# Kernel optimization log

Hardware: AMD Instinct MI355X
Metric: run time of the kernel (lower is better)

Reference implementation:

```python
import jax, jax.numpy as jnp
import numpy as np

INF = jnp.float32(1e9)  # sentinel; true costs are O(10)


def _hungarian_cost(cost):
    """Exact min-cost perfect matching total cost (Jonker-Volgenant potentials
    algorithm, O(n^3)), matching scipy.optimize.linear_sum_assignment.
    cost: (n, n) float32 -> scalar sum of matched costs."""
    n = cost.shape[0]
    # pad with dummy row/col 0 (1-indexed algorithm)
    a = jnp.zeros((n + 1, n + 1), cost.dtype).at[1:, 1:].set(cost)

    def row_step(carry, i):
        u, v, p = carry  # u,v: dual potentials; p[j] = row matched to col j
        p = p.at[0].set(i)
        minv = jnp.full(n + 1, INF, cost.dtype)
        used = jnp.zeros(n + 1, bool)
        way = jnp.zeros(n + 1, jnp.int32)

        def cond(st):
            u, v, p, minv, used, way, j0, first = st
            return first | (p[j0] != 0)

        def body(st):
            u, v, p, minv, used, way, j0, _ = st
            used = used.at[j0].set(True)
            i0 = p[j0]
            cur = a[i0] - u[i0] - v                      # reduced costs of row i0
            upd = (~used) & (cur < minv)
            way = jnp.where(upd, j0, way)
            minv = jnp.where(upd, cur, minv)
            masked = jnp.where(used, INF, minv)
            j1 = jnp.argmin(masked).astype(jnp.int32)
            delta = masked[j1]
            # u[p[j]] += delta for used j (unused scatter adds 0, harmless)
            u = u.at[p].add(jnp.where(used, delta, 0.0))
            v = jnp.where(used, v - delta, v)
            minv = jnp.where(used, minv, minv - delta)
            return (u, v, p, minv, used, way, j1, False)

        u, v, p, minv, used, way, j0, _ = jax.lax.while_loop(
            cond, body, (u, v, p, minv, used, way, jnp.int32(0), True))

        # augment along alternating path
        def aug_body(st):
            p, j0 = st
            j1 = way[j0]
            return p.at[j0].set(p[j1]), j1

        p, _ = jax.lax.while_loop(lambda st: st[1] != 0, aug_body, (p, j0))
        return (u, v, p), None

    init = (jnp.zeros(n + 1, cost.dtype),
            jnp.zeros(n + 1, cost.dtype),
            jnp.zeros(n + 1, jnp.int32))
    (u, v, p), _ = jax.lax.scan(row_step, init,
                                jnp.arange(1, n + 1, dtype=jnp.int32))
    cols = jnp.arange(1, n + 1)
    return a[p[1:], cols].sum()


def setup_inputs() -> dict:
    key = jax.random.key(0)
    k1, k2 = jax.random.split(key)
    B, N = 8, 1024
    S1 = jax.random.normal(k1, (B, N, 3), dtype=jnp.float32)
    S2 = jax.random.normal(k2, (B, N, 3), dtype=jnp.float32)
    return {"S1": S1, "S2": S2}


def reference(S1, S2):
    B, N, _ = S1.shape
    # torch.cdist(p=2): per-sample pairwise Euclidean distances -> (B, N, N)
    diff = S1[:, :, None, :] - S2[:, None, :, :]
    cost = jnp.sqrt(jnp.sum(diff * diff, axis=-1))
    per_sample = jax.vmap(_hungarian_cost)(cost) / N  # optimal assignment cost / N
    return jnp.mean(per_sample)
```

## Files before the change

kernel.cpp:

```cpp
#include <hip/hip_runtime.h>
#include <hip/hip_fp16.h>
#include <math.h>


#define N     1024
#define BATCH 8
#define NSLOT 16
#define INFV  1e9f
#define AUC_ROUNDS 48

__global__ void emd_zero_kernel(float* out) { out[0] = 0.0f; }

__global__ __launch_bounds__(256)
void emd_dist_kernel(const float* __restrict__ S1, const float* __restrict__ S2,
                     __half* __restrict__ D) {
    int b = blockIdx.x >> 10;
    int r = blockIdx.x & (N - 1);
    const float* s1 = S1 + ((size_t)b * N + r) * 3;
    float x1 = s1[0], y1 = s1[1], z1 = s1[2];
    const float* s2 = S2 + (size_t)b * N * 3;
    __half* drow = D + ((size_t)b * N + r) * (size_t)N;
    for (int c = threadIdx.x; c < N; c += 256) {
        float dx = x1 - s2[3 * c], dy = y1 - s2[3 * c + 1], dz = z1 - s2[3 * c + 2];
        drow[c] = __float2half_rn(sqrtf(dx * dx + dy * dy + dz * dz));
    }
}

__global__ __launch_bounds__(256)
void emd_colmin_kernel(const __half* __restrict__ D, float* __restrict__ V,
                       int* __restrict__ I) {
    int b = blockIdx.x >> 2;
    int c = ((blockIdx.x & 3) << 8) + threadIdx.x;
    const __half* Db = D + ((size_t)b << 20);
    float best = INFV; int bi = 1;
    for (int r = 0; r < N; ++r) {
        float d = __half2float(Db[(size_t)r * N + c]);
        if (d < best) { best = d; bi = r + 1; }
    }
    V[b * N + c] = best;
    I[b * N + c] = bi;
}

template<int CTRL>
__device__ __forceinline__ float dppmin(float x) {
    int xi = __float_as_int(x);
    int yi = __builtin_amdgcn_update_dpp(xi, xi, CTRL, 0xF, 0xF, false);
    return fminf(x, __int_as_float(yi));
}

__device__ __forceinline__ float wave_min_f32(float x) {
    x = dppmin<0x111>(x);
    x = dppmin<0x112>(x);
    x = dppmin<0x114>(x);
    x = dppmin<0x118>(x);
    x = dppmin<0x142>(x);
    x = dppmin<0x143>(x);
    return __int_as_float(__builtin_amdgcn_readlane(__float_as_int(x), 63));
}

__global__ __launch_bounds__(1024, 1)
void emd_auction_kernel(const __half* __restrict__ Dc,
                        const float* __restrict__ Vin,
                        const int* __restrict__ Iin,
                        float* __restrict__ Vw, float* __restrict__ Uw,
                        int* __restrict__ Cw, int* __restrict__ Rw) {
    __shared__ float v0[N];
    __shared__ int   rowm[N + 1];
    __shared__ int   colm[N + 1];
    __shared__ unsigned long long bid[N + 1];
    __shared__ int   qbuf[N];
    __shared__ int   qn;

    const int tid  = threadIdx.x;
    const int lane = tid & 63;
    const int wv   = tid >> 6;
    const int b    = blockIdx.x;
    const __half* Db = Dc + ((size_t)b << 20);

    for (int t = tid; t <= N; t += 1024) { rowm[t] = 0; colm[t] = 0; bid[t] = 0ull; }
    for (int c = tid; c < N; c += 1024) v0[c] = Vin[b * N + c];
    __syncthreads();

    for (int c = tid; c < N; c += 1024) {
        int r = Iin[b * N + c];
        int old = atomicCAS(&rowm[r], 0, c + 1);
        if (old == 0) colm[c + 1] = r;
    }
    __syncthreads();

    auto rowRed16 = [&](int i, float (&red)[16]) {
        const uint4* dr = (const uint4*)(Db + (size_t)(i - 1) * N);
        uint4 w0 = dr[lane * 2 + 0];
        uint4 w1 = dr[lane * 2 + 1];
        unsigned wb[8] = { w0.x, w0.y, w0.z, w0.w, w1.x, w1.y, w1.z, w1.w };
        const float4* vp = (const float4*)(v0 + lane * 16);
        float4 vv0 = vp[0], vv1 = vp[1], vv2 = vp[2], vv3 = vp[3];
        float vv[16] = { vv0.x, vv0.y, vv0.z, vv0.w, vv1.x, vv1.y, vv1.z, vv1.w,
                         vv2.x, vv2.y, vv2.z, vv2.w, vv3.x, vv3.y, vv3.z, vv3.w };
#pragma unroll
        for (int t = 0; t < 8; ++t) {
            __half2 hh = *reinterpret_cast<const __half2*>(&wb[t]);
            float2 f2 = __half22float2(hh);
            red[2 * t]     = f2.x - vv[2 * t];
            red[2 * t + 1] = f2.y - vv[2 * t + 1];
        }
    };

    for (int round = 0; round < AUC_ROUNDS; ++round) {
        if (tid == 0) qn = 0;
        __syncthreads();
        for (int i = tid + 1; i <= N; i += 1024)
            if (rowm[i] == 0) { int p = atomicAdd(&qn, 1); qbuf[p] = i; }
        __syncthreads();
        int nq = qn;
        if (nq == 0) break;

        for (int q = wv; q < nq; q += 16) {
            int i = qbuf[q];
            float red[16];
            rowRed16(i, red);
            float a1 = INFV, a2 = INFV; int ac = 0;
            float e1 = INFV, e2 = INFV; int ec = 0;
            float f1 = INFV, f2 = INFV; int fc = 0;
            float g1 = INFV, g2 = INFV; int gc = 0;
#pragma unroll
            for (int k = 0; k < 4; ++k) {
                float u0 = red[k];
                bool t0 = u0 < a1;
                a2 = t0 ? a1 : (u0 < a2 ? u0 : a2);
                ac = t0 ? (lane * 16 + k) : ac;  a1 = t0 ? u0 : a1;
                float u1 = red[k + 4];
                bool t1 = u1 < e1;
                e2 = t1 ? e1 : (u1 < e2 ? u1 : e2);
                ec = t1 ? (lane * 16 + k + 4) : ec;  e1 = t1 ? u1 : e1;
                float u2 = red[k + 8];
                bool t2 = u2 < f1;
                f2 = t2 ? f1 : (u2 < f2 ? u2 : f2);
                fc = t2 ? (lane * 16 + k + 8) : fc;  f1 = t2 ? u2 : f1;
                float u3 = red[k + 12];
                bool t3 = u3 < g1;
                g2 = t3 ? g1 : (u3 < g2 ? u3 : g2);
                gc = t3 ? (lane * 16 + k + 12) : gc;  g1 = t3 ? u3 : g1;
            }
            bool sae = e1 < a1;
            float ae1 = sae ? e1 : a1; int aec = sae ? ec : ac;
            float ae2 = fminf(fminf(a2, e2), sae ? a1 : e1);
            bool sfg = g1 < f1;
            float fg1 = sfg ? g1 : f1; int fgc = sfg ? gc : fc;
            float fg2 = fminf(fminf(f2, g2), sfg ? f1 : g1);
            bool sall = fg1 < ae1;
            float m1 = sall ? fg1 : ae1;
            int   c1 = sall ? fgc : aec;
            float m2 = fminf(fminf(ae2, fg2), sall ? ae1 : fg1);

            float gm1 = wave_min_f32(m1);
            unsigned long long wbm = __ballot(m1 == gm1);
            int wl = __ffsll((long long)wbm) - 1;
            float cand2 = (lane == wl) ? m2 : m1;
            float gm2 = wave_min_f32(cand2);
            int gcol;
            if (gm1 < gm2) {
                gcol = __builtin_amdgcn_readlane(c1, wl);
            } else {
                unsigned tmask = 0u;
#pragma unroll
                for (int k = 0; k < 16; ++k)
                    tmask |= (red[k] == gm1) ? (1u << k) : 0u;
                unsigned fmask = 0u;
                unsigned tt = tmask;
                while (tt) {
                    int k = __ffs((int)tt) - 1;
                    tt &= tt - 1;
                    if (colm[lane * 16 + k + 1] == 0) fmask |= (1u << k);
                }
                unsigned long long bf = __ballot(fmask != 0u);
                if (bf != 0ull) {
                    int l = __ffsll((long long)bf) - 1;
                    unsigned mk = (unsigned)__builtin_amdgcn_readlane((int)fmask, l);
                    gcol = l * 16 + (__ffs((int)mk) - 1);
                } else {
                    gcol = __builtin_amdgcn_readlane(c1, wl);
                }
            }
            float inc = gm2 - gm1;

            if (lane == 0) {
                unsigned long long key =
                    ((unsigned long long)__float_as_uint(inc) << 32) |
                    (unsigned long long)(unsigned)i;
                atomicMax(&bid[gcol + 1], key);
            }
        }
        __syncthreads();

        for (int j = tid + 1; j <= N; j += 1024) {
            unsigned long long bb = bid[j];
            if (bb != 0ull) {
                bid[j] = 0ull;
                int i = (int)(unsigned)(bb & 0xFFFFFFFFull);
                float inc = __uint_as_float((unsigned)(bb >> 32));
                int old = colm[j];
                colm[j] = i;
                rowm[i] = j;
                if (old) rowm[old] = 0;
                v0[j - 1] -= inc;
            }
        }
        __syncthreads();
    }

    for (int q = wv; q < N; q += 16) {
        int i = q + 1;
        float red[16];
        rowRed16(i, red);
        int j = rowm[i];
        float rloc = red[0];
        int lo = 0, kk = 0;
        if (j) {
            lo = (j - 1) >> 4; kk = (j - 1) & 15;
#pragma unroll
            for (int k = 1; k < 16; ++k) if (k == kk) rloc = red[k];
        }
#pragma unroll
        for (int s = 1; s < 16; s <<= 1) {
#pragma unroll
            for (int k = 0; k < 16; k += 2 * s)
                red[k] = fminf(red[k], red[k + s]);
        }
        float m = wave_min_f32(red[0]);
        if (j) {
            float rm = __int_as_float(
                __builtin_amdgcn_readlane(__float_as_int(rloc), lo));
            if (lane == 0 && rm != m) { rowm[i] = 0; colm[j] = 0; }
        }
        if (lane == 0) Uw[b * N + q] = m;
    }
    __syncthreads();

    for (int c = tid; c < N; c += 1024) {
        Vw[b * N + c] = v0[c];
        Cw[b * N + c] = colm[c + 1];
    }
    for (int t = tid; t < N; t += 1024) Rw[b * N + t] = rowm[t + 1];
}

struct Frag { uint4 w0, w1; float ur; float4 q; };

template<bool CACHED, bool PRE>
__global__ __launch_bounds__(64, 1)
void emd_jv_kernel(const float* __restrict__ S1,
                   const float* __restrict__ S2,
                   const __half* __restrict__ Dc,
                   const float* __restrict__ Vin,
                   const int*   __restrict__ Iin,
                   const float* __restrict__ Uw,
                   const int*   __restrict__ Cw,
                   const int*   __restrict__ Rw,
                   float* __restrict__ out) {
    __shared__ float4 s1u[N + 1];
    __shared__ float  u_lds[N + 1];
    __shared__ float  dentry[N + 1];
    __shared__ int    rowm[N + 1];

    const int lane = threadIdx.x;
    const int b = blockIdx.x;
    const float* s1g = S1 + (size_t)b * N * 3;
    const float* s2g = S2 + (size_t)b * N * 3;
    const __half* Db = CACHED ? (Dc + ((size_t)b << 20)) : (const __half*)0;
    const float NANF = __int_as_float(0x7fc00000);

    for (int t = lane; t < N; t += 64) {
        s1u[t + 1] = make_float4(s1g[3 * t], s1g[3 * t + 1], s1g[3 * t + 2], 0.0f);
        u_lds[t + 1] = PRE ? Uw[b * N + t] : 0.0f;
        rowm[t + 1] = PRE ? Rw[b * N + t] : 0;
    }
    if (lane == 0) { u_lds[0] = 0.0f; rowm[0] = 0; }

    float v[NSLOT];
    int   pr[NSLOT];
    int   jpk[NSLOT];
    float x2[NSLOT], y2[NSLOT], z2[NSLOT];

#pragma unroll
    for (int k = 0; k < NSLOT; ++k) {
        int pt = lane * NSLOT + k;
        x2[k] = s2g[3 * pt + 0];
        y2[k] = s2g[3 * pt + 1];
        z2[k] = s2g[3 * pt + 2];
    }

    if constexpr (PRE) {
#pragma unroll
        for (int k = 0; k < NSLOT; ++k) {
            int c = lane * NSLOT + k;
            v[k] = Vin[b * N + c];
            pr[k] = Cw[b * N + c];
            jpk[k] = (pr[k] << 11) | (c + 1);
        }
        __syncthreads();
    } else {
        int imin[NSLOT];
        if constexpr (CACHED) {
#pragma unroll
            for (int k = 0; k < NSLOT; ++k) {
                int c = lane * NSLOT + k;
                v[k] = Vin[b * N + c];
                imin[k] = Iin[b * N + c];
            }
        } else {
#pragma unroll
            for (int k = 0; k < NSLOT; ++k) { v[k] = INFV; imin[k] = 1; }
        }
        __syncthreads();

        if constexpr (!CACHED) {
            for (int r = 1; r <= N; ++r) {
                float4 qq = s1u[r];
#pragma unroll
                for (int k = 0; k < NSLOT; ++k) {
                    float dx = qq.x - x2[k], dy = qq.y - y2[k], dz = qq.z - z2[k];
                    float d2 = dx * dx + dy * dy + dz * dz;
                    bool upd = d2 < v[k];
                    v[k] = upd ? d2 : v[k];
                    imin[k] = upd ? r : imin[k];
                }
            }
#pragma unroll
            for (int k = 0; k < NSLOT; ++k) v[k] = sqrtf(v[k]);
        }

#pragma unroll
        for (int k = 0; k < NSLOT; ++k) {
            int j = lane * NSLOT + k + 1;
            int r = imin[k];
            int old = atomicCAS(&rowm[r], 0, j);
            pr[k] = (old == 0) ? r : 0;
            jpk[k] = (pr[k] << 11) | j;
        }
        __syncthreads();
    }

    float minv[NSLOT];
    int   way[NSLOT];

    auto issueLoads = [&](int rr) -> Frag {
        Frag F;
        if (CACHED) {
            const uint4* dr = (const uint4*)(Db + (size_t)(rr - 1) * N);
            F.w0 = dr[lane * 2 + 0];
            F.w1 = dr[lane * 2 + 1];
        } else {
            F.q = s1u[rr];
        }
        F.ur = u_lds[rr];
        return F;
    };

    auto applyFrag = [&](const Frag& F, int jpred, float Dh) {
        float base = Dh - F.ur;
        if (CACHED) {
            float h[NSLOT];
            const unsigned* w = (const unsigned*)&F.w0;
#pragma unroll
            for (int t = 0; t < 8; ++t) {
                unsigned word = w[t];
                __half2 hh = *reinterpret_cast<const __half2*>(&word);
                float2 f2 = __half22float2(hh);
                h[2 * t] = f2.x; h[2 * t + 1] = f2.y;
            }
#pragma unroll
            for (int k = 0; k < NSLOT; ++k) {
                float cur = (h[k] - v[k]) + base;
                bool upd = cur < minv[k];
                minv[k] = upd ? cur : minv[k];
                way[k] = upd ? jpred : way[k];
            }
        } else {
#pragma unroll
            for (int k = 0; k < NSLOT; ++k) {
                float dx = F.q.x - x2[k], dy = F.q.y - y2[k], dz = F.q.z - z2[k];
                float d = sqrtf(dx * dx + dy * dy + dz * dz);
                float cur = (d - v[k]) + base;
                bool upd = cur < minv[k];
                minv[k] = upd ? cur : minv[k];
                way[k] = upd ? jpred : way[k];
            }
        }
    };

    for (int i = 1; i <= N; ++i) {
        if (rowm[i] != 0) continue;

        unsigned used = 0u;
        float DT = 0.0f;
        int freecol = 0;
        int pred = 0;
        Frag P;

        Frag F0 = issueLoads(i);
#pragma unroll
        for (int k = 0; k < NSLOT; ++k) { minv[k] = INFV; way[k] = 0; }
        applyFrag(F0, 0, 0.0f);

        int guard = 0;
        for (;;) {
            if (++guard > N + 4) break;
            float b0 = INFV, b1 = INFV, b2 = INFV, b3 = INFV;
            int   p0 = 0, p1 = 0, p2 = 0, p3 = 0;
#pragma unroll
            for (int k = 0; k < 4; ++k) {
                bool t0 = minv[k]      < b0;
                b0 = t0 ? minv[k]      : b0;  p0 = t0 ? jpk[k]      : p0;
                bool t1 = minv[k + 4]  < b1;
                b1 = t1 ? minv[k + 4]  : b1;  p1 = t1 ? jpk[k + 4]  : p1;
                bool t2 = minv[k + 8]  < b2;
                b2 = t2 ? minv[k + 8]  : b2;  p2 = t2 ? jpk[k + 8]  : p2;
                bool t3 = minv[k + 12] < b3;
                b3 = t3 ? minv[k + 12] : b3;  p3 = t3 ? jpk[k + 12] : p3;
            }
            bool m01 = b1 < b0;  float ba = m01 ? b1 : b0;  int pa = m01 ? p1 : p0;
            bool m23 = b3 < b2;  float bb = m23 ? b3 : b2;  int pb = m23 ? p3 : p2;
            bool mab = bb < ba;  float bestv = mab ? bb : ba;
            int bestjp = mab ? pb : pa;

            float gmin = wave_min_f32(bestv);
            if (!(gmin < INFV * 0.5f)) break;
            unsigned long long tm = __ballot(bestv == gmin);
            DT = gmin;
            freecol = 0;

            {
                unsigned long long tf = tm;
                while (tf) {
                    int l = __ffsll((long long)tf) - 1;
                    tf &= tf - 1;
                    int jp = __builtin_amdgcn_readlane(bestjp, l);
                    if ((jp >> 11) == 0) { freecol = jp & 0x7FF; break; }
                }
            }
            if (freecol) break;

            bool first = true;
            while (tm) {
                int l = __ffsll((long long)tm) - 1;
                tm &= tm - 1;
                int jp = __builtin_amdgcn_readlane(bestjp, l);
                int jj = jp & 0x7FF, rr = jp >> 11;
                Frag F;
                if (CACHED && first && pred != 0 && rr == pred) {
                    F = P;
                } else {
                    F = issueLoads(rr);
                }
                if (CACHED && first) {
                    float ru = (bestv == gmin) ? INFV : bestv;
                    float rmin = wave_min_f32(ru);
                    pred = 0;
                    if (rmin < INFV * 0.5f) {
                        unsigned long long rb = __ballot(ru == rmin);
                        int rl = __ffsll((long long)rb) - 1;
                        int rjp = __builtin_amdgcn_readlane(bestjp, rl);
                        int prr = rjp >> 11;
                        if (prr != 0) { pred = prr; P = issueLoads(prr); }
                    }
                }
                first = false;
                if (lane == 0) dentry[jj] = gmin;
                int cc = jj - 1, lo = cc >> 4, kk = cc & 15;
                bool mine = (lane == lo);
#pragma unroll
                for (int k = 0; k < NSLOT; ++k)
                    if (k == kk && mine) { minv[k] = NANF; used |= (1u << k); }
                applyFrag(F, jj, gmin);
            }
        }
        if (freecol == 0) continue;

        if (lane == 0) u_lds[i] += DT;
#pragma unroll
        for (int k = 0; k < NSLOT; ++k) {
            if ((used >> k) & 1u) {
                int j = lane * NSLOT + k + 1;
                float dd = DT - dentry[j];
                v[k] -= dd;
                u_lds[pr[k]] += dd;
            }
        }
        __syncthreads();

        int j0 = freecol;
        int aguard = 0;
        while (j0 != 0) {
            if (++aguard > N + 4) break;
            int cc = j0 - 1;
            int lo = cc >> 4, kk = cc & 15;
            int wloc = way[0];
#pragma unroll
            for (int k = 1; k < NSLOT; ++k) if (k == kk) wloc = way[k];
            int j1 = __builtin_amdgcn_readlane(wloc, lo);
            int np;
            if (j1 == 0) np = i;
            else {
                int c1 = j1 - 1;
                int lo1 = c1 >> 4, kk1 = c1 & 15;
                int ploc = pr[0];
#pragma unroll
                for (int k = 1; k < NSLOT; ++k) if (k == kk1) ploc = pr[k];
                np = __builtin_amdgcn_readlane(ploc, lo1);
            }
            bool mine = (lane == lo);
#pragma unroll
            for (int k = 0; k < NSLOT; ++k)
                if (k == kk) {
                    if (mine) { pr[k] = np; jpk[k] = (np << 11) | j0; }
                }
            if (lane == 0) rowm[np] = j0;
            j0 = j1;
        }
        __syncthreads();
    }

    float sum = 0.0f;
#pragma unroll
    for (int k = 0; k < NSLOT; ++k) {
        int r = pr[k] > 0 ? pr[k] : 1;
        float4 qq = s1u[r];
        float dx = qq.x - x2[k], dy = qq.y - y2[k], dz = qq.z - z2[k];
        sum += sqrtf(dx * dx + dy * dy + dz * dz);
    }
#pragma unroll
    for (int off = 32; off >= 1; off >>= 1) sum += __shfl_xor(sum, off);
    if (lane == 0) atomicAdd(out, sum * (1.0f / ((float)N * (float)BATCH)));
}

extern "C" void kernel_launch(void* const* d_in, const int* in_sizes, int n_in,
                              void* d_out, int out_size, void* d_ws, size_t ws_size,
                              hipStream_t stream) {
    const float* S1 = (const float*)d_in[0];
    const float* S2 = (const float*)d_in[1];
    float* out = (float*)d_out;

    size_t needD  = (size_t)BATCH * N * N * sizeof(__half);
    size_t vecB   = (size_t)BATCH * N * 4;
    size_t needT  = needD + 2 * vecB;
    size_t needT2 = needD + 6 * vecB;

    emd_zero_kernel<<<1, 1, 0, stream>>>(out);

    if (ws_size >= needT2) {
        __half* D  = (__half*)d_ws;
        float*  V  = (float*)((char*)d_ws + needD);
        int*    I  = (int*)((char*)V + vecB);
        float*  Vw = (float*)((char*)I + vecB);
        float*  Uw = (float*)((char*)Vw + vecB);
        int*    Cw = (int*)((char*)Uw + vecB);
        int*    Rw = (int*)((char*)Cw + vecB);
        emd_dist_kernel<<<BATCH * N, 256, 0, stream>>>(S1, S2, D);
        emd_colmin_kernel<<<BATCH * 4, 256, 0, stream>>>(D, V, I);
        emd_auction_kernel<<<BATCH, 1024, 0, stream>>>(D, V, I, Vw, Uw, Cw, Rw);
        emd_jv_kernel<true, true><<<BATCH, 64, 0, stream>>>(
            S1, S2, D, Vw, nullptr, Uw, Cw, Rw, out);
    } else if (ws_size >= needT) {
        __half* D = (__half*)d_ws;
        float*  V = (float*)((char*)d_ws + needD);
        int*    I = (int*)((char*)V + vecB);
        emd_dist_kernel<<<BATCH * N, 256, 0, stream>>>(S1, S2, D);
        emd_colmin_kernel<<<BATCH * 4, 256, 0, stream>>>(D, V, I);
        emd_jv_kernel<true, false><<<BATCH, 64, 0, stream>>>(
            S1, S2, D, V, I, nullptr, nullptr, nullptr, out);
    } else {
        emd_jv_kernel<false, false><<<BATCH, 64, 0, stream>>>(
            S1, S2, nullptr, nullptr, nullptr, nullptr, nullptr, nullptr, out);
    }
}
```

Baseline: 17.81 ms.

## Add second auction phase after evicting non-tight assignments, alternate tie-breaking

Splits the auction warm-start into two phases. After the first batch of rounds, each assigned row is checked for whether its column is still a reduced-cost minimum, and non-tight assignments are evicted. A second, shorter batch of auction rounds then re-matches the freed rows. On odd rounds, ties with no free column are now broken by picking the highest-index tied column, to reduce bidding conflicts. The aim is a larger, tighter initial matching so the exact Hungarian augmentation afterwards has less work, at the cost of extra rounds and a full row scan.

```diff
diff --git a/kernel.cpp b/kernel.cpp
--- a/kernel.cpp
+++ b/kernel.cpp
@@ -7,7 +7,8 @@
 #define BATCH 8
 #define NSLOT 16
 #define INFV  1e9f
-#define AUC_ROUNDS 48
+#define AUC_R1 48
+#define AUC_R2 24
 
 __global__ void emd_zero_kernel(float* out) { out[0] = 0.0f; }
 
@@ -106,108 +107,142 @@
         }
     };
 
-    for (int round = 0; round < AUC_ROUNDS; ++round) {
-        if (tid == 0) qn = 0;
-        __syncthreads();
-        for (int i = tid + 1; i <= N; i += 1024)
-            if (rowm[i] == 0) { int p = atomicAdd(&qn, 1); qbuf[p] = i; }
-        __syncthreads();
-        int nq = qn;
-        if (nq == 0) break;
-
-        for (int q = wv; q < nq; q += 16) {
-            int i = qbuf[q];
-            float red[16];
-            rowRed16(i, red);
-            float a1 = INFV, a2 = INFV; int ac = 0;
-            float e1 = INFV, e2 = INFV; int ec = 0;
-            float f1 = INFV, f2 = INFV; int fc = 0;
-            float g1 = INFV, g2 = INFV; int gc = 0;
-#pragma unroll
-            for (int k = 0; k < 4; ++k) {
-                float u0 = red[k];
-                bool t0 = u0 < a1;
-                a2 = t0 ? a1 : (u0 < a2 ? u0 : a2);
-                ac = t0 ? (lane * 16 + k) : ac;  a1 = t0 ? u0 : a1;
-                float u1 = red[k + 4];
-                bool t1 = u1 < e1;
-                e2 = t1 ? e1 : (u1 < e2 ? u1 : e2);
-                ec = t1 ? (lane * 16 + k + 4) : ec;  e1 = t1 ? u1 : e1;
-                float u2 = red[k + 8];
-                bool t2 = u2 < f1;
-                f2 = t2 ? f1 : (u2 < f2 ? u2 : f2);
-                fc = t2 ? (lane * 16 + k + 8) : fc;  f1 = t2 ? u2 : f1;
-                float u3 = red[k + 12];
-                bool t3 = u3 < g1;
-                g2 = t3 ? g1 : (u3 < g2 ? u3 : g2);
-                gc = t3 ? (lane * 16 + k + 12) : gc;  g1 = t3 ? u3 : g1;
-            }
-            bool sae = e1 < a1;
-            float ae1 = sae ? e1 : a1; int aec = sae ? ec : ac;
-            float ae2 = fminf(fminf(a2, e2), sae ? a1 : e1);
-            bool sfg = g1 < f1;
-            float fg1 = sfg ? g1 : f1; int fgc = sfg ? gc : fc;
-            float fg2 = fminf(fminf(f2, g2), sfg ? f1 : g1);
-            bool sall = fg1 < ae1;
-            float m1 = sall ? fg1 : ae1;
-            int   c1 = sall ? fgc : aec;
-            float m2 = fminf(fminf(ae2, fg2), sall ? ae1 : fg1);
-
-            float gm1 = wave_min_f32(m1);
-            unsigned long long wbm = __ballot(m1 == gm1);
-            int wl = __ffsll((long long)wbm) - 1;
-            float cand2 = (lane == wl) ? m2 : m1;
-            float gm2 = wave_min_f32(cand2);
-            int gcol;
-            if (gm1 < gm2) {
-                gcol = __builtin_amdgcn_readlane(c1, wl);
-            } else {
-                unsigned tmask = 0u;
-#pragma unroll
-                for (int k = 0; k < 16; ++k)
-                    tmask |= (red[k] == gm1) ? (1u << k) : 0u;
-                unsigned fmask = 0u;
-                unsigned tt = tmask;
-                while (tt) {
-                    int k = __ffs((int)tt) - 1;
-                    tt &= tt - 1;
-                    if (colm[lane * 16 + k + 1] == 0) fmask |= (1u << k);
-                }
-                unsigned long long bf = __ballot(fmask != 0u);
-                if (bf != 0ull) {
-                    int l = __ffsll((long long)bf) - 1;
-                    unsigned mk = (unsigned)__builtin_amdgcn_readlane((int)fmask, l);
-                    gcol = l * 16 + (__ffs((int)mk) - 1);
+    auto runRounds = [&](int nrounds) {
+        for (int round = 0; round < nrounds; ++round) {
+            if (tid == 0) qn = 0;
+            __syncthreads();
+            for (int i = tid + 1; i <= N; i += 1024)
+                if (rowm[i] == 0) { int p = atomicAdd(&qn, 1); qbuf[p] = i; }
+            __syncthreads();
+            int nq = qn;
+            if (nq == 0) break;
+
+            for (int q = wv; q < nq; q += 16) {
+                int i = qbuf[q];
+                float red[16];
+                rowRed16(i, red);
+                float a1 = INFV, a2 = INFV; int ac = 0;
+                float e1 = INFV, e2 = INFV; int ec = 0;
+                float f1 = INFV, f2 = INFV; int fc = 0;
+                float g1 = INFV, g2 = INFV; int gc = 0;
+#pragma unroll
+                for (int k = 0; k < 4; ++k) {
+                    float u0 = red[k];
+                    bool t0 = u0 < a1;
+                    a2 = t0 ? a1 : (u0 < a2 ? u0 : a2);
+                    ac = t0 ? (lane * 16 + k) : ac;  a1 = t0 ? u0 : a1;
+                    float u1 = red[k + 4];
+                    bool t1 = u1 < e1;
+                    e2 = t1 ? e1 : (u1 < e2 ? u1 : e2);
+                    ec = t1 ? (lane * 16 + k + 4) : ec;  e1 = t1 ? u1 : e1;
+                    float u2 = red[k + 8];
+                    bool t2 = u2 < f1;
+                    f2 = t2 ? f1 : (u2 < f2 ? u2 : f2);
+                    fc = t2 ? (lane * 16 + k + 8) : fc;  f1 = t2 ? u2 : f1;
+                    float u3 = red[k + 12];
+                    bool t3 = u3 < g1;
+                    g2 = t3 ? g1 : (u3 < g2 ? u3 : g2);
+                    gc = t3 ? (lane * 16 + k + 12) : gc;  g1 = t3 ? u3 : g1;
+                }
+                bool sae = e1 < a1;
+                float ae1 = sae ? e1 : a1; int aec = sae ? ec : ac;
+                float ae2 = fminf(fminf(a2, e2), sae ? a1 : e1);
+                bool sfg = g1 < f1;
+                float fg1 = sfg ? g1 : f1; int fgc = sfg ? gc : fc;
+                float fg2 = fminf(fminf(f2, g2), sfg ? f1 : g1);
+                bool sall = fg1 < ae1;
+                float m1 = sall ? fg1 : ae1;
+                int   c1 = sall ? fgc : aec;
+                float m2 = fminf(fminf(ae2, fg2), sall ? ae1 : fg1);
+
+                float gm1 = wave_min_f32(m1);
+                unsigned long long wbm = __ballot(m1 == gm1);
+                int wl = __ffsll((long long)wbm) - 1;
+                float cand2 = (lane == wl) ? m2 : m1;
+                float gm2 = wave_min_f32(cand2);
+                int gcol;
+                if (gm1 < gm2) {
+                    gcol = __builtin_amdgcn_readlane(c1, wl);
                 } else {
-                    gcol = __builtin_amdgcn_readlane(c1, wl);
-                }
-            }
-            float inc = gm2 - gm1;
-
-            if (lane == 0) {
-                unsigned long long key =
-                    ((unsigned long long)__float_as_uint(inc) << 32) |
-                    (unsigned long long)(unsigned)i;
-                atomicMax(&bid[gcol + 1], key);
-            }
-        }
-        __syncthreads();
-
-        for (int j = tid + 1; j <= N; j += 1024) {
-            unsigned long long bb = bid[j];
-            if (bb != 0ull) {
-                bid[j] = 0ull;
-                int i = (int)(unsigned)(bb & 0xFFFFFFFFull);
-                float inc = __uint_as_float((unsigned)(bb >> 32));
-                int old = colm[j];
-                colm[j] = i;
-                rowm[i] = j;
-                if (old) rowm[old] = 0;
-                v0[j - 1] -= inc;
-            }
-        }
-        __syncthreads();
-    }
+                    unsigned tmask = 0u;
+#pragma unroll
+                    for (int k = 0; k < 16; ++k)
+                        tmask |= (red[k] == gm1) ? (1u << k) : 0u;
+                    unsigned fmask = 0u;
+                    unsigned tt = tmask;
+                    while (tt) {
+                        int k = __ffs((int)tt) - 1;
+                        tt &= tt - 1;
+                        if (colm[lane * 16 + k + 1] == 0) fmask |= (1u << k);
+                    }
+                    unsigned long long bf = __ballot(fmask != 0u);
+                    if (bf != 0ull) {
+                        int l = __ffsll((long long)bf) - 1;
+                        unsigned mk = (unsigned)__builtin_amdgcn_readlane((int)fmask, l);
+                        gcol = l * 16 + (__ffs((int)mk) - 1);
+                    } else if (round & 1) {
+                        unsigned long long ba = __ballot(tmask != 0u);
+                        int l = 63 - __clzll(ba);
+                        unsigned mk = (unsigned)__builtin_amdgcn_readlane((int)tmask, l);
+                        gcol = l * 16 + (31 - __clz((int)mk));
+                    } else {
+                        gcol = __builtin_amdgcn_readlane(c1, wl);
+                    }
+                }
+                float inc = gm2 - gm1;
+
+                if (lane == 0) {
+                    unsigned long long key =
+                        ((unsigned long long)__float_as_uint(inc) << 32) |
+                        (unsigned long long)(unsigned)i;
+                    atomicMax(&bid[gcol + 1], key);
+                }
+            }
+            __syncthreads();
+
+            for (int j = tid + 1; j <= N; j += 1024) {
+                unsigned long long bb = bid[j];
+                if (bb != 0ull) {
+                    bid[j] = 0ull;
+                    int i = (int)(unsigned)(bb & 0xFFFFFFFFull);
+                    float inc = __uint_as_float((unsigned)(bb >> 32));
+                    int old = colm[j];
+                    colm[j] = i;
+                    rowm[i] = j;
+                    if (old) rowm[old] = 0;
+                    v0[j - 1] -= inc;
+                }
+            }
+            __syncthreads();
+        }
+    };
+
+    runRounds(AUC_R1);
+
+    for (int q = wv; q < N; q += 16) {
+        int i = q + 1;
+        int j = rowm[i];
+        if (j == 0) continue;
+        float red[16];
+        rowRed16(i, red);
+        int lo = (j - 1) >> 4, kk = (j - 1) & 15;
+        float rloc = red[0];
+#pragma unroll
+        for (int k = 1; k < 16; ++k) if (k == kk) rloc = red[k];
+#pragma unroll
+        for (int s = 1; s < 16; s <<= 1) {
+#pragma unroll
+            for (int k = 0; k < 16; k += 2 * s)
+                red[k] = fminf(red[k], red[k + s]);
+        }
+        float m = wave_min_f32(red[0]);
+        float rm = __int_as_float(
+            __builtin_amdgcn_readlane(__float_as_int(rloc), lo));
+        if (lane == 0 && rm != m) { rowm[i] = 0; colm[j] = 0; }
+    }
+    __syncthreads();
+
+    runRounds(AUC_R2);
 
     for (int q = wv; q < N; q += 16) {
         int i = q + 1;
```

Result: faster. 17.37 ms (-2.5%).
